# Performance work log

Hardware: AMD Instinct MI355X
Metric: run time of the kernel (lower is better)

Reference implementation:

```python
import jax, jax.numpy as jnp
import numpy as np

N = 100000       # nodes
E = 1600000      # edges (avg degree 16)
D = 128          # features_dim = hidden_dim = out_dim
G = 3            # group_num
NUM = 50000      # nodes present in all time groups
ALPHA = 0.2      # LeakyReLU slope
W_SCALE = 0.05


def setup_inputs() -> dict:
    key = jax.random.key(0)
    ks = jax.random.split(key, 8)
    x = jax.random.normal(ks[0], (N, D), jnp.float32)
    edge_index = jax.random.randint(ks[1], (2, E), 0, N, dtype=jnp.int64)
    past = jax.random.normal(ks[2], (G - 1, NUM, D), jnp.float32)
    W1 = jax.random.normal(ks[3], (2 * D, D), jnp.float32) * W_SCALE
    W2 = jax.random.normal(ks[4], (2 * D, D), jnp.float32) * W_SCALE
    W0 = jax.random.normal(ks[5], (D, D), jnp.float32) * W_SCALE
    Wp = jax.random.normal(ks[6], (G - 1, D, D), jnp.float32) * W_SCALE
    W_T = jax.random.normal(ks[7], (2 * D, D), jnp.float32) * W_SCALE
    return {"x": x, "past": past, "W1": W1, "W2": W2, "W0": W0,
            "Wp": Wp, "W_T": W_T, "edge_index": edge_index, "num": NUM}


def reference(x, past, W1, W2, W0, Wp, W_T, edge_index, num):
    src, dst = edge_index[0], edge_index[1]
    n = x.shape[0]
    deg = jax.ops.segment_sum(jnp.ones(src.shape[0], x.dtype), dst, num_segments=n)
    deg = jnp.maximum(deg, 1.0)[:, None]

    def sage_layer(h, W):
        # mean-aggregate neighbors, concat with self, linear + ReLU
        agg = jax.ops.segment_sum(h[src], dst, num_segments=n) / deg
        return jax.nn.relu(jnp.concatenate([h, agg], axis=1) @ W)

    feat = sage_layer(x, W1)      # [N, D]
    feat = sage_layer(feat, W2)   # [N, D]

    # temporal mean aggregation (dropout is identity in eval mode)
    time_feat = (feat[:num] @ W0 + jnp.einsum('knd,kde->ne', past, Wp)) / G
    fused = jnp.concatenate([feat[:num], time_feat], axis=1) @ W_T  # [num, D]
    f = jax.nn.leaky_relu(fused, ALPHA)
    f = f / jnp.maximum(jnp.linalg.norm(f, axis=1, keepdims=True), 1e-12)
    return jnp.concatenate([f, feat[num:]], axis=0)  # [N, D]
```

## Files before the change

### kernel.cpp

```cpp
#include <hip/hip_runtime.h>

#define FD 128
#define CAP 64
#define BSH 8
#define MAXNB 512

typedef __attribute__((ext_vector_type(8))) short bf16x8;
typedef __attribute__((ext_vector_type(4))) float f32x4;

__device__ __forceinline__ float bflo(unsigned v) { return __uint_as_float(v << 16); }
__device__ __forceinline__ float bfhi(unsigned v) { return __uint_as_float(v & 0xffff0000u); }
__device__ __forceinline__ unsigned short f2b(float f) {
  unsigned u = __float_as_uint(f);
  return (unsigned short)((u + 0x7fffu + ((u >> 16) & 1u)) >> 16);
}
__device__ __forceinline__ unsigned pack2(float x, float y) {
  return (unsigned)f2b(x) | ((unsigned)f2b(y) << 16);
}

#if __has_builtin(__builtin_amdgcn_fdot2_f32_bf16)
#define HAVE_DOT2 1
typedef __attribute__((ext_vector_type(2))) __bf16 bf16x2;
__device__ __forceinline__ float dot2acc(unsigned v, unsigned w, float acc) {
  return __builtin_amdgcn_fdot2_f32_bf16(__builtin_bit_cast(bf16x2, v),
                                         __builtin_bit_cast(bf16x2, w), acc, false);
}
#endif

__global__ __launch_bounds__(256) void k_hist(const int* __restrict__ dst,
                                              int* __restrict__ binCnt, int E, int n, int NB) {
  __shared__ int lh[MAXNB];
  for (int i = threadIdx.x; i < NB; i += 256) lh[i] = 0;
  __syncthreads();
  for (int e = blockIdx.x * 256 + threadIdx.x; e < E; e += gridDim.x * 256) {
    unsigned d = (unsigned)dst[e];
    if (d < (unsigned)n) atomicAdd(&lh[d >> BSH], 1);
  }
  __syncthreads();
  for (int i = threadIdx.x; i < NB; i += 256) {
    int c = lh[i];
    if (c) atomicAdd(&binCnt[i], c);
  }
}

__global__ __launch_bounds__(512) void k_scan(const int* __restrict__ binCnt,
                                              int* __restrict__ binStart,
                                              int* __restrict__ binCur, int NB) {
  __shared__ int buf[512];
  int t = threadIdx.x;
  int v0 = (t < NB) ? binCnt[t] : 0;
  buf[t] = v0;
  __syncthreads();
  for (int off = 1; off < 512; off <<= 1) {
    int v = (t >= off) ? buf[t - off] : 0;
    __syncthreads();
    buf[t] += v;
    __syncthreads();
  }
  if (t < NB) {
    int ex = buf[t] - v0;
    binStart[t] = ex;
    binCur[t] = ex;
  }
}

__global__ __launch_bounds__(256) void k_binscatter(const int* __restrict__ src,
                                                    const int* __restrict__ dst,
                                                    int* __restrict__ binCur,
                                                    unsigned* __restrict__ binned, int E, int n, int NB) {
  __shared__ int lcnt[MAXNB], lbase[MAXNB];
  const int CH = 4096;
  int e0 = blockIdx.x * CH;
  for (int i = threadIdx.x; i < NB; i += 256) lcnt[i] = 0;
  __syncthreads();
  int se[16], de[16];
#pragma unroll
  for (int k = 0; k < 16; ++k) {
    int e = e0 + k * 256 + threadIdx.x;
    int ok = e < E;
    unsigned s = ok ? (unsigned)src[e] : 0u;
    unsigned d = ok ? (unsigned)dst[e] : 0u;
    if (s >= (unsigned)n) s = 0;
    ok = ok && d < (unsigned)n;
    se[k] = (int)s;
    de[k] = ok ? (int)d : -1;
    if (ok) atomicAdd(&lcnt[d >> BSH], 1);
  }
  __syncthreads();
  for (int i = threadIdx.x; i < NB; i += 256) {
    int c = lcnt[i];
    lbase[i] = c ? atomicAdd(&binCur[i], c) : 0;
    lcnt[i] = 0;
  }
  __syncthreads();
#pragma unroll
  for (int k = 0; k < 16; ++k) {
    if (de[k] >= 0) {
      int b = de[k] >> BSH;
      int p = lbase[b] + atomicAdd(&lcnt[b], 1);
      binned[p] = ((unsigned)(de[k] & 255) << 24) | (unsigned)se[k];
    }
  }
}

__global__ __launch_bounds__(256) void k_bucket2(const unsigned* __restrict__ binned,
                                                 const int* __restrict__ binStart,
                                                 const int* __restrict__ binCnt,
                                                 int* __restrict__ cnt,
                                                 int* __restrict__ idx, int n) {
  __shared__ int lcnt[256];
  int bin = blockIdx.x;
  int base = bin << BSH;
  lcnt[threadIdx.x] = 0;
  __syncthreads();
  int s0 = binStart[bin], c0 = binCnt[bin];
  for (int i = threadIdx.x; i < c0; i += 256) {
    unsigned pr = binned[s0 + i];
    int dlow = (int)(pr >> 24);
    int p = atomicAdd(&lcnt[dlow], 1);
    if (p < CAP) idx[(size_t)(base + dlow) * CAP + p] = (int)(pr & 0xFFFFFFu);
  }
  __syncthreads();
  int d = base + threadIdx.x;
  if (d < n) cnt[d] = lcnt[threadIdx.x];
}

__global__ __launch_bounds__(256) void k_xcast(const float4* __restrict__ x,
                                               unsigned short* __restrict__ xb, int total4) {
  int i = blockIdx.x * 256 + threadIdx.x;
  if (i >= total4) return;
  float4 v = x[i];
  *(uint2*)&xb[(size_t)i * 4] = make_uint2(pack2(v.x, v.y), pack2(v.z, v.w));
}

__global__ __launch_bounds__(64) void k_wpack(const float* __restrict__ W,
                                              unsigned short* __restrict__ Wf, int KROWS) {
  int nkt = KROWS >> 5;
  int ct = blockIdx.x % 8, kt = blockIdx.x / 8;
  int lane = threadIdx.x;
  int m = lane & 15, q = lane >> 4;
  int nn = ct * 16 + m;
  int k0 = kt * 32 + q * 8;
  unsigned short tmp[8];
#pragma unroll
  for (int j = 0; j < 8; ++j) tmp[j] = f2b(W[(size_t)(k0 + j) * FD + nn]);
  unsigned short* dst = Wf + ((size_t)(ct * nkt + kt) * 64 + lane) * 8;
  *(uint4*)dst = *(uint4*)tmp;
}

__global__ __launch_bounds__(64) void k_wpack3(const float* __restrict__ W0,
                                               const float* __restrict__ WpA,
                                               const float* __restrict__ WpB,
                                               unsigned short* __restrict__ Wf) {
  int ct = blockIdx.x % 8, kt = blockIdx.x / 8;
  const float* src = kt < 4 ? W0 : (kt < 8 ? WpA : WpB);
  int ktl = kt & 3;
  int lane = threadIdx.x;
  int m = lane & 15, q = lane >> 4;
  int nn = ct * 16 + m;
  int k0 = ktl * 32 + q * 8;
  unsigned short tmp[8];
#pragma unroll
  for (int j = 0; j < 8; ++j) tmp[j] = f2b(src[(size_t)(k0 + j) * FD + nn]);
  unsigned short* dst = Wf + ((size_t)(ct * 12 + kt) * 64 + lane) * 8;
  *(uint4*)dst = *(uint4*)tmp;
}

__global__ __launch_bounds__(256) void k_sage(const unsigned* __restrict__ hb,
                                              const int* __restrict__ cnt,
                                              const int* __restrict__ idx,
                                              const unsigned short* __restrict__ Wf,
                                              float* __restrict__ outf,
                                              unsigned short* __restrict__ outb,
                                              int nbThr, int n) {
  __shared__ unsigned short sa[32][264];
  int tid = threadIdx.x;
  int lane = tid & 63, wv = tid >> 6;
  int rowBase = blockIdx.x * 32;

  for (int i = tid; i < 32 * 32; i += 256) {
    int r = i >> 5, cp = i & 31;
    int gr = rowBase + r;
    uint2 v = (gr < n) ? *(const uint2*)&hb[(size_t)gr * 64 + cp * 2] : make_uint2(0u, 0u);
    *(uint2*)&sa[r][cp * 4] = v;
  }

  int rbase = wv * 8;
  const int* ip = idx + (size_t)(rowBase + rbase) * CAP;
  int vidx[8];
  int c[8];
  int maxc = 0;
#pragma unroll
  for (int j = 0; j < 8; ++j) {
    int gr = rowBase + rbase + j;
    int cj = (gr < n) ? min(cnt[gr], CAP) : 0;
    cj = __builtin_amdgcn_readfirstlane(cj);
    c[j] = cj;
    maxc = max(maxc, cj);
    int v = 0;
    if (lane < cj) v = ip[j * CAP + lane];
    vidx[j] = v;
  }

#ifdef HAVE_DOT2
  float sxa[8], dxa[8];
#pragma unroll
  for (int j = 0; j < 8; ++j) { sxa[j] = 0.f; dxa[j] = 0.f; }
  const unsigned ONES = 0x3F803F80u;
  const unsigned PMON = 0xBF803F80u;

  for (int e = 0; e < maxc; e += 4) {
    int l1 = min(e + 1, CAP - 1), l2 = min(e + 2, CAP - 1), l3 = min(e + 3, CAP - 1);
    unsigned v[8][4];
#pragma unroll
    for (int j = 0; j < 8; ++j) {
      int s0 = __builtin_amdgcn_readlane(vidx[j], e);
      int s1 = __builtin_amdgcn_readlane(vidx[j], l1);
      int s2 = __builtin_amdgcn_readlane(vidx[j], l2);
      int s3 = __builtin_amdgcn_readlane(vidx[j], l3);
      s0 = (e     < c[j]) ? s0 : n;
      s1 = (e + 1 < c[j]) ? s1 : n;
      s2 = (e + 2 < c[j]) ? s2 : n;
      s3 = (e + 3 < c[j]) ? s3 : n;
      v[j][0] = hb[(size_t)s0 * 64 + lane];
      v[j][1] = hb[(size_t)s1 * 64 + lane];
      v[j][2] = hb[(size_t)s2 * 64 + lane];
      v[j][3] = hb[(size_t)s3 * 64 + lane];
    }
#pragma unroll
    for (int j = 0; j < 8; ++j) {
#pragma unroll
      for (int k = 0; k < 4; ++k) {
        sxa[j] = dot2acc(v[j][k], ONES, sxa[j]);
        dxa[j] = dot2acc(v[j][k], PMON, dxa[j]);
      }
    }
  }
#pragma unroll
  for (int j = 0; j < 8; ++j) {
    float inv = 0.5f / fmaxf((float)c[j], 1.0f);
    float ax = (sxa[j] + dxa[j]) * inv;
    float ay = (sxa[j] - dxa[j]) * inv;
    *(unsigned*)&sa[rbase + j][FD + lane * 2] = pack2(ax, ay);
  }
#else
  float ax[8], ay[8];
#pragma unroll
  for (int j = 0; j < 8; ++j) { ax[j] = 0.f; ay[j] = 0.f; }

  for (int e = 0; e < maxc; e += 4) {
    int l1 = min(e + 1, CAP - 1), l2 = min(e + 2, CAP - 1), l3 = min(e + 3, CAP - 1);
    unsigned v[8][4];
#pragma unroll
    for (int j = 0; j < 8; ++j) {
      int s0 = __builtin_amdgcn_readlane(vidx[j], e);
      int s1 = __builtin_amdgcn_readlane(vidx[j], l1);
      int s2 = __builtin_amdgcn_readlane(vidx[j], l2);
      int s3 = __builtin_amdgcn_readlane(vidx[j], l3);
      s0 = (e     < c[j]) ? s0 : n;
      s1 = (e + 1 < c[j]) ? s1 : n;
      s2 = (e + 2 < c[j]) ? s2 : n;
      s3 = (e + 3 < c[j]) ? s3 : n;
      v[j][0] = hb[(size_t)s0 * 64 + lane];
      v[j][1] = hb[(size_t)s1 * 64 + lane];
      v[j][2] = hb[(size_t)s2 * 64 + lane];
      v[j][3] = hb[(size_t)s3 * 64 + lane];
    }
#pragma unroll
    for (int j = 0; j < 8; ++j) {
#pragma unroll
      for (int k = 0; k < 4; ++k) {
        ax[j] += bflo(v[j][k]);
        ay[j] += bfhi(v[j][k]);
      }
    }
  }
#pragma unroll
  for (int j = 0; j < 8; ++j) {
    float inv = 1.0f / fmaxf((float)c[j], 1.0f);
    *(unsigned*)&sa[rbase + j][FD + lane * 2] = pack2(ax[j] * inv, ay[j] * inv);
  }
#endif
  __syncthreads();

  int m = lane & 15, q = lane >> 4;
  f32x4 z = {0.f, 0.f, 0.f, 0.f};
  f32x4 acc[2][2] = {{z, z}, {z, z}};
  int ct0 = wv * 2;
  const bf16x8* WfV = (const bf16x8*)Wf;
#pragma unroll
  for (int kt = 0; kt < 8; ++kt) {
    bf16x8 a0 = *(const bf16x8*)&sa[m][kt * 32 + q * 8];
    bf16x8 a1 = *(const bf16x8*)&sa[16 + m][kt * 32 + q * 8];
    bf16x8 b0 = WfV[(size_t)(ct0 * 8 + kt) * 64 + lane];
    bf16x8 b1 = WfV[(size_t)((ct0 + 1) * 8 + kt) * 64 + lane];
    acc[0][0] = __builtin_amdgcn_mfma_f32_16x16x32_bf16(a0, b0, acc[0][0], 0, 0, 0);
    acc[0][1] = __builtin_amdgcn_mfma_f32_16x16x32_bf16(a0, b1, acc[0][1], 0, 0, 0);
    acc[1][0] = __builtin_amdgcn_mfma_f32_16x16x32_bf16(a1, b0, acc[1][0], 0, 0, 0);
    acc[1][1] = __builtin_amdgcn_mfma_f32_16x16x32_bf16(a1, b1, acc[1][1], 0, 0, 0);
  }

#pragma unroll
  for (int rt = 0; rt < 2; ++rt) {
#pragma unroll
    for (int t = 0; t < 2; ++t) {
      int col = (ct0 + t) * 16 + m;
#pragma unroll
      for (int reg = 0; reg < 4; ++reg) {
        int gr = rowBase + rt * 16 + q * 4 + reg;
        if (gr < n) {
          float v = fmaxf(acc[rt][t][reg], 0.f);
          if (gr < nbThr)
            outb[(size_t)gr * FD + col] = f2b(v);
          else
            outf[(size_t)gr * FD + col] = v;
        }
      }
    }
  }
}

__global__ __launch_bounds__(256) void k_fuse(const unsigned short* __restrict__ feat2b,
                                              const float* __restrict__ past,
                                              const unsigned short* __restrict__ Wcf,
                                              const unsigned short* __restrict__ Wtf,
                                              float* __restrict__ out, int num) {
  __shared__ unsigned short sa[32][392];
  __shared__ float so[32][132];
  int tid = threadIdx.x;
  int lane = tid & 63, wv = tid >> 6;
  int base = blockIdx.x * 32;

  const unsigned* f2u = (const unsigned*)feat2b;
  for (int i = tid; i < 32 * 64; i += 256) {
    int r = i >> 6, cp = i & 63;
    int gr = base + r;
    unsigned uvf = 0u;
    float2 v0 = {0.f, 0.f}, v1 = {0.f, 0.f};
    if (gr < num) {
      uvf = f2u[(size_t)gr * 64 + cp];
      v0 = *(const float2*)&past[(size_t)gr * FD + cp * 2];
      v1 = *(const float2*)&past[(size_t)num * FD + (size_t)gr * FD + cp * 2];
    }
    *(unsigned*)&sa[r][cp * 2]       = uvf;
    *(unsigned*)&sa[r][FD + cp * 2]  = pack2(v0.x, v0.y);
    *(unsigned*)&sa[r][256 + cp * 2] = pack2(v1.x, v1.y);
  }
  __syncthreads();

  int m = lane & 15, q = lane >> 4;
  int ct0 = wv * 2;
  f32x4 z = {0.f, 0.f, 0.f, 0.f};
  const bf16x8* WcV = (const bf16x8*)Wcf;
  const bf16x8* WtV = (const bf16x8*)Wtf;

  f32x4 acc[2][2] = {{z, z}, {z, z}};
#pragma unroll
  for (int kt = 0; kt < 12; ++kt) {
    bf16x8 a0 = *(const bf16x8*)&sa[m][kt * 32 + q * 8];
    bf16x8 a1 = *(const bf16x8*)&sa[16 + m][kt * 32 + q * 8];
    bf16x8 b0 = WcV[(size_t)(ct0 * 12 + kt) * 64 + lane];
    bf16x8 b1 = WcV[(size_t)((ct0 + 1) * 12 + kt) * 64 + lane];
    acc[0][0] = __builtin_amdgcn_mfma_f32_16x16x32_bf16(a0, b0, acc[0][0], 0, 0, 0);
    acc[0][1] = __builtin_amdgcn_mfma_f32_16x16x32_bf16(a0, b1, acc[0][1], 0, 0, 0);
    acc[1][0] = __builtin_amdgcn_mfma_f32_16x16x32_bf16(a1, b0, acc[1][0], 0, 0, 0);
    acc[1][1] = __builtin_amdgcn_mfma_f32_16x16x32_bf16(a1, b1, acc[1][1], 0, 0, 0);
  }
  __syncthreads();

  const float inv3 = 1.0f / 3.0f;
#pragma unroll
  for (int rt = 0; rt < 2; ++rt)
#pragma unroll
    for (int t = 0; t < 2; ++t) {
      int col = (ct0 + t) * 16 + m;
#pragma unroll
      for (int reg = 0; reg < 4; ++reg)
        sa[rt * 16 + q * 4 + reg][FD + col] = f2b(acc[rt][t][reg] * inv3);
    }
  __syncthreads();

  f32x4 acc2[2][2] = {{z, z}, {z, z}};
#pragma unroll
  for (int kt = 0; kt < 8; ++kt) {
    bf16x8 a0 = *(const bf16x8*)&sa[m][kt * 32 + q * 8];
    bf16x8 a1 = *(const bf16x8*)&sa[16 + m][kt * 32 + q * 8];
    bf16x8 b0 = WtV[(size_t)(ct0 * 8 + kt) * 64 + lane];
    bf16x8 b1 = WtV[(size_t)((ct0 + 1) * 8 + kt) * 64 + lane];
    acc2[0][0] = __builtin_amdgcn_mfma_f32_16x16x32_bf16(a0, b0, acc2[0][0], 0, 0, 0);
    acc2[0][1] = __builtin_amdgcn_mfma_f32_16x16x32_bf16(a0, b1, acc2[0][1], 0, 0, 0);
    acc2[1][0] = __builtin_amdgcn_mfma_f32_16x16x32_bf16(a1, b0, acc2[1][0], 0, 0, 0);
    acc2[1][1] = __builtin_amdgcn_mfma_f32_16x16x32_bf16(a1, b1, acc2[1][1], 0, 0, 0);
  }

#pragma unroll
  for (int rt = 0; rt < 2; ++rt)
#pragma unroll
    for (int t = 0; t < 2; ++t) {
      int col = (ct0 + t) * 16 + m;
#pragma unroll
      for (int reg = 0; reg < 4; ++reg) {
        float v = acc2[rt][t][reg];
        so[rt * 16 + q * 4 + reg][col] = v > 0.f ? v : 0.2f * v;
      }
    }
  __syncthreads();

#pragma unroll
  for (int j = 0; j < 8; ++j) {
    int r = wv * 8 + j;
    float v0 = so[r][lane * 2], v1 = so[r][lane * 2 + 1];
    float ss = v0 * v0 + v1 * v1;
#pragma unroll
    for (int mk = 32; mk >= 1; mk >>= 1) ss += __shfl_xor(ss, mk, 64);
    float inv = 1.0f / fmaxf(sqrtf(ss), 1e-12f);
    int gr = base + r;
    if (gr < num) {
      float2 o = {v0 * inv, v1 * inv};
      *(float2*)&out[(size_t)gr * FD + lane * 2] = o;
    }
  }
}

extern "C" void kernel_launch(void* const* d_in, const int* in_sizes, int n_in,
                              void* d_out, int out_size, void* d_ws, size_t ws_size,
                              hipStream_t stream) {
  const float* x    = (const float*)d_in[0];
  const float* past = (const float*)d_in[1];
  const float* W1   = (const float*)d_in[2];
  const float* W2   = (const float*)d_in[3];
  const float* W0   = (const float*)d_in[4];
  const float* Wp   = (const float*)d_in[5];
  const float* WT   = (const float*)d_in[6];
  const int*   ei   = (const int*)d_in[7];

  int N   = in_sizes[0] / FD;
  int NUM = in_sizes[1] / (2 * FD);
  int E   = in_sizes[7] / 2;
  const int* src = ei;
  const int* dst = ei + E;
  float* out = (float*)d_out;

  int NB = (N + 255) >> BSH;

  char* p = (char*)d_ws;
  int* cnt      = (int*)p;  p += (((size_t)N * 4 + 255) & ~(size_t)255);
  int* idx      = (int*)p;  p += (size_t)N * CAP * 4;
  int* binCnt   = (int*)p;  p += MAXNB * 4;
  int* binStart = (int*)p;  p += MAXNB * 4;
  int* binCur   = (int*)p;  p += MAXNB * 4;
  unsigned* binned = (unsigned*)p; p += (size_t)E * 4;
  unsigned short* xb  = (unsigned short*)p; p += (size_t)(N + 1) * FD * 2;
  unsigned short* f1b = (unsigned short*)p; p += (size_t)(N + 1) * FD * 2;
  unsigned short* w1f = (unsigned short*)p; p += (size_t)8 * 8 * 64 * 8 * 2;
  unsigned short* w2f = (unsigned short*)p; p += (size_t)8 * 8 * 64 * 8 * 2;
  unsigned short* wcf = (unsigned short*)p; p += (size_t)8 * 12 * 64 * 8 * 2;
  unsigned short* wtf = (unsigned short*)p;
  unsigned short* f2b = xb;

  hipMemsetAsync(binCnt, 0, MAXNB * sizeof(int), stream);
  hipMemsetAsync(xb + (size_t)N * FD, 0, FD * 2, stream);
  hipMemsetAsync(f1b + (size_t)N * FD, 0, FD * 2, stream);

  k_hist<<<400, 256, 0, stream>>>(dst, binCnt, E, N, NB);
  k_scan<<<1, 512, 0, stream>>>(binCnt, binStart, binCur, NB);
  k_binscatter<<<(E + 4095) / 4096, 256, 0, stream>>>(src, dst, binCur, binned, E, N, NB);
  k_bucket2<<<NB, 256, 0, stream>>>(binned, binStart, binCnt, cnt, idx, N);

  k_xcast<<<(N * 32 + 255) / 256, 256, 0, stream>>>((const float4*)x, xb, N * 32);
  k_wpack<<<64, 64, 0, stream>>>(W1, w1f, 2 * FD);
  k_wpack<<<64, 64, 0, stream>>>(W2, w2f, 2 * FD);
  k_wpack3<<<96, 64, 0, stream>>>(W0, Wp, Wp + FD * FD, wcf);
  k_wpack<<<64, 64, 0, stream>>>(WT, wtf, 2 * FD);

  int sageGrid = (N + 31) / 32;
  k_sage<<<sageGrid, 256, 0, stream>>>((const unsigned*)xb, cnt, idx, w1f, nullptr, f1b, N, N);
  k_sage<<<sageGrid, 256, 0, stream>>>((const unsigned*)f1b, cnt, idx, w2f, out, f2b, NUM, N);
  k_fuse<<<(NUM + 31) / 32, 256, 0, stream>>>(f2b, past, wcf, wtf, out, NUM);
}
```

Before: 400.4 us.

## Merge preprocessing kernels and fold bin scan into scatter and bucket kernels

Merges the x-to-bf16 cast, the destination histogram, all weight packing and the padding-row zeroing into one multi-role prep kernel, replacing several small launches and two memsets. The separate scan kernel is removed: each binscatter and bucket block recomputes the prefix sum of bin counts in shared memory. Bin size grows from 256 to 512 destinations, halving the number of bins and changing the packed edge encoding to a 9-bit local id. This cuts launch count and serialization gaps, at the cost of redundant per-block scans and fewer, larger bucket blocks.

```diff
diff --git a/kernel.cpp b/kernel.cpp
--- a/kernel.cpp
+++ b/kernel.cpp
@@ -2,8 +2,9 @@
 
 #define FD 128
 #define CAP 64
-#define BSH 8
-#define MAXNB 512
+#define BSH 9
+#define BINSZ 512
+#define NBMAX 256
 
 typedef __attribute__((ext_vector_type(8))) short bf16x8;
 typedef __attribute__((ext_vector_type(4))) float f32x4;
@@ -27,56 +28,115 @@
 }
 #endif
 
-__global__ __launch_bounds__(256) void k_hist(const int* __restrict__ dst,
-                                              int* __restrict__ binCnt, int E, int n, int NB) {
-  __shared__ int lh[MAXNB];
-  for (int i = threadIdx.x; i < NB; i += 256) lh[i] = 0;
-  __syncthreads();
-  for (int e = blockIdx.x * 256 + threadIdx.x; e < E; e += gridDim.x * 256) {
-    unsigned d = (unsigned)dst[e];
-    if (d < (unsigned)n) atomicAdd(&lh[d >> BSH], 1);
-  }
-  __syncthreads();
-  for (int i = threadIdx.x; i < NB; i += 256) {
-    int c = lh[i];
-    if (c) atomicAdd(&binCnt[i], c);
-  }
-}
-
-__global__ __launch_bounds__(512) void k_scan(const int* __restrict__ binCnt,
-                                              int* __restrict__ binStart,
-                                              int* __restrict__ binCur, int NB) {
-  __shared__ int buf[512];
+__device__ __forceinline__ void wpack_tile(const float* __restrict__ W,
+                                           unsigned short* __restrict__ Wf,
+                                           int nkt, int tt, int lane) {
+  int ct = tt & 7, kt = tt >> 3;
+  int m = lane & 15, q = lane >> 4;
+  int nn = ct * 16 + m;
+  int k0 = kt * 32 + q * 8;
+  unsigned short tmp[8];
+#pragma unroll
+  for (int j = 0; j < 8; ++j) tmp[j] = f2b(W[(size_t)(k0 + j) * FD + nn]);
+  unsigned short* dst = Wf + ((size_t)(ct * nkt + kt) * 64 + lane) * 8;
+  *(uint4*)dst = *(uint4*)tmp;
+}
+
+__global__ __launch_bounds__(256) void k_prep(const float4* __restrict__ x4,
+                                              unsigned short* __restrict__ xb, int total4,
+                                              const int* __restrict__ dst,
+                                              int* __restrict__ binCnt, int E, int n, int NB,
+                                              const float* __restrict__ W1,
+                                              const float* __restrict__ W2,
+                                              const float* __restrict__ W0,
+                                              const float* __restrict__ Wp,
+                                              const float* __restrict__ WT,
+                                              unsigned short* __restrict__ w1f,
+                                              unsigned short* __restrict__ w2f,
+                                              unsigned short* __restrict__ wcf,
+                                              unsigned short* __restrict__ wtf,
+                                              unsigned short* __restrict__ f1b,
+                                              int XCB, int HB) {
+  __shared__ int lh[NBMAX];
+  int b = blockIdx.x, tid = threadIdx.x;
+
+  if (b < XCB) {
+    int i = b * 256 + tid;
+    if (i < total4) {
+      float4 v = x4[i];
+      *(uint2*)&xb[(size_t)i * 4] = make_uint2(pack2(v.x, v.y), pack2(v.z, v.w));
+    }
+    return;
+  }
+  b -= XCB;
+  if (b < HB) {
+    for (int i = tid; i < NB; i += 256) lh[i] = 0;
+    __syncthreads();
+    for (int e = b * 256 + tid; e < E; e += HB * 256) {
+      unsigned d = (unsigned)dst[e];
+      if (d < (unsigned)n) atomicAdd(&lh[d >> BSH], 1);
+    }
+    __syncthreads();
+    for (int i = tid; i < NB; i += 256) {
+      int c = lh[i];
+      if (c) atomicAdd(&binCnt[i], c);
+    }
+    return;
+  }
+  b -= HB;
+  if (b < 72) {
+    int t4 = b * 4 + (tid >> 6);
+    int lane = tid & 63;
+    if (t4 < 64) wpack_tile(W1, w1f, 8, t4, lane);
+    else if (t4 < 128) wpack_tile(W2, w2f, 8, t4 - 64, lane);
+    else if (t4 < 192) wpack_tile(WT, wtf, 8, t4 - 128, lane);
+    else {
+      int tt = t4 - 192;
+      int ct = tt & 7, kt = tt >> 3;
+      const float* src = kt < 4 ? W0 : (kt < 8 ? Wp : (Wp + FD * FD));
+      int ktl = kt & 3;
+      int m = lane & 15, q = lane >> 4;
+      int nn = ct * 16 + m;
+      int k0 = ktl * 32 + q * 8;
+      unsigned short tmp[8];
+#pragma unroll
+      for (int j = 0; j < 8; ++j) tmp[j] = f2b(src[(size_t)(k0 + j) * FD + nn]);
+      unsigned short* dstp = wcf + ((size_t)(ct * 12 + kt) * 64 + lane) * 8;
+      *(uint4*)dstp = *(uint4*)tmp;
+    }
+    return;
+  }
+  if (tid < 64) ((unsigned*)&xb[(size_t)n * FD])[tid] = 0u;
+  else if (tid < 128) ((unsigned*)&f1b[(size_t)n * FD])[tid - 64] = 0u;
+}
+
+__global__ __launch_bounds__(256) void k_binscatter(const int* __restrict__ src,
+                                                    const int* __restrict__ dst,
+                                                    const int* __restrict__ binCnt,
+                                                    int* __restrict__ binCur,
+                                                    unsigned* __restrict__ binned,
+                                                    int E, int n, int NB) {
+  __shared__ int sbuf[NBMAX], sstart[NBMAX], lcnt[NBMAX], lbase[NBMAX];
   int t = threadIdx.x;
   int v0 = (t < NB) ? binCnt[t] : 0;
-  buf[t] = v0;
-  __syncthreads();
-  for (int off = 1; off < 512; off <<= 1) {
-    int v = (t >= off) ? buf[t - off] : 0;
+  sbuf[t] = v0;
+  __syncthreads();
+  for (int off = 1; off < 256; off <<= 1) {
+    int v = (t >= off) ? sbuf[t - off] : 0;
     __syncthreads();
-    buf[t] += v;
+    sbuf[t] += v;
     __syncthreads();
   }
-  if (t < NB) {
-    int ex = buf[t] - v0;
-    binStart[t] = ex;
-    binCur[t] = ex;
-  }
-}
-
-__global__ __launch_bounds__(256) void k_binscatter(const int* __restrict__ src,
-                                                    const int* __restrict__ dst,
-                                                    int* __restrict__ binCur,
-                                                    unsigned* __restrict__ binned, int E, int n, int NB) {
-  __shared__ int lcnt[MAXNB], lbase[MAXNB];
+  sstart[t] = sbuf[t] - v0;
+  lcnt[t] = 0;
+  __syncthreads();
+
   const int CH = 4096;
   int e0 = blockIdx.x * CH;
-  for (int i = threadIdx.x; i < NB; i += 256) lcnt[i] = 0;
-  __syncthreads();
   int se[16], de[16];
 #pragma unroll
   for (int k = 0; k < 16; ++k) {
-    int e = e0 + k * 256 + threadIdx.x;
+    int e = e0 + k * 256 + t;
     int ok = e < E;
     unsigned s = ok ? (unsigned)src[e] : 0u;
     unsigned d = ok ? (unsigned)dst[e] : 0u;
@@ -87,83 +147,56 @@
     if (ok) atomicAdd(&lcnt[d >> BSH], 1);
   }
   __syncthreads();
-  for (int i = threadIdx.x; i < NB; i += 256) {
+  for (int i = t; i < NB; i += 256) {
     int c = lcnt[i];
-    lbase[i] = c ? atomicAdd(&binCur[i], c) : 0;
+    lbase[i] = c ? (sstart[i] + atomicAdd(&binCur[i], c)) : 0;
     lcnt[i] = 0;
   }
   __syncthreads();
 #pragma unroll
   for (int k = 0; k < 16; ++k) {
     if (de[k] >= 0) {
-      int b = de[k] >> BSH;
-      int p = lbase[b] + atomicAdd(&lcnt[b], 1);
-      binned[p] = ((unsigned)(de[k] & 255) << 24) | (unsigned)se[k];
+      int bb = de[k] >> BSH;
+      int p = lbase[bb] + atomicAdd(&lcnt[bb], 1);
+      binned[p] = ((unsigned)(de[k] & (BINSZ - 1)) << 23) | (unsigned)se[k];
     }
   }
 }
 
 __global__ __launch_bounds__(256) void k_bucket2(const unsigned* __restrict__ binned,
-                                                 const int* __restrict__ binStart,
                                                  const int* __restrict__ binCnt,
                                                  int* __restrict__ cnt,
-                                                 int* __restrict__ idx, int n) {
-  __shared__ int lcnt[256];
-  int bin = blockIdx.x;
+                                                 int* __restrict__ idx, int n, int NB) {
+  __shared__ int sbuf[NBMAX];
+  __shared__ int lcnt[BINSZ];
+  int bin = blockIdx.x, t = threadIdx.x;
+  int v0 = (t < NB) ? binCnt[t] : 0;
+  sbuf[t] = v0;
+  __syncthreads();
+  for (int off = 1; off < 256; off <<= 1) {
+    int v = (t >= off) ? sbuf[t - off] : 0;
+    __syncthreads();
+    sbuf[t] += v;
+    __syncthreads();
+  }
+  int c0 = binCnt[bin];
+  int s0 = sbuf[bin] - c0;
+  lcnt[t] = 0;
+  lcnt[t + 256] = 0;
+  __syncthreads();
+
   int base = bin << BSH;
-  lcnt[threadIdx.x] = 0;
-  __syncthreads();
-  int s0 = binStart[bin], c0 = binCnt[bin];
-  for (int i = threadIdx.x; i < c0; i += 256) {
+  for (int i = t; i < c0; i += 256) {
     unsigned pr = binned[s0 + i];
-    int dlow = (int)(pr >> 24);
+    int dlow = (int)(pr >> 23);
     int p = atomicAdd(&lcnt[dlow], 1);
-    if (p < CAP) idx[(size_t)(base + dlow) * CAP + p] = (int)(pr & 0xFFFFFFu);
-  }
-  __syncthreads();
-  int d = base + threadIdx.x;
-  if (d < n) cnt[d] = lcnt[threadIdx.x];
-}
-
-__global__ __launch_bounds__(256) void k_xcast(const float4* __restrict__ x,
-                                               unsigned short* __restrict__ xb, int total4) {
-  int i = blockIdx.x * 256 + threadIdx.x;
-  if (i >= total4) return;
-  float4 v = x[i];
-  *(uint2*)&xb[(size_t)i * 4] = make_uint2(pack2(v.x, v.y), pack2(v.z, v.w));
-}
-
-__global__ __launch_bounds__(64) void k_wpack(const float* __restrict__ W,
-                                              unsigned short* __restrict__ Wf, int KROWS) {
-  int nkt = KROWS >> 5;
-  int ct = blockIdx.x % 8, kt = blockIdx.x / 8;
-  int lane = threadIdx.x;
-  int m = lane & 15, q = lane >> 4;
-  int nn = ct * 16 + m;
-  int k0 = kt * 32 + q * 8;
-  unsigned short tmp[8];
-#pragma unroll
-  for (int j = 0; j < 8; ++j) tmp[j] = f2b(W[(size_t)(k0 + j) * FD + nn]);
-  unsigned short* dst = Wf + ((size_t)(ct * nkt + kt) * 64 + lane) * 8;
-  *(uint4*)dst = *(uint4*)tmp;
-}
-
-__global__ __launch_bounds__(64) void k_wpack3(const float* __restrict__ W0,
-                                               const float* __restrict__ WpA,
-                                               const float* __restrict__ WpB,
-                                               unsigned short* __restrict__ Wf) {
-  int ct = blockIdx.x % 8, kt = blockIdx.x / 8;
-  const float* src = kt < 4 ? W0 : (kt < 8 ? WpA : WpB);
-  int ktl = kt & 3;
-  int lane = threadIdx.x;
-  int m = lane & 15, q = lane >> 4;
-  int nn = ct * 16 + m;
-  int k0 = ktl * 32 + q * 8;
-  unsigned short tmp[8];
-#pragma unroll
-  for (int j = 0; j < 8; ++j) tmp[j] = f2b(src[(size_t)(k0 + j) * FD + nn]);
-  unsigned short* dst = Wf + ((size_t)(ct * 12 + kt) * 64 + lane) * 8;
-  *(uint4*)dst = *(uint4*)tmp;
+    if (p < CAP) idx[(size_t)(base + dlow) * CAP + p] = (int)(pr & 0x7FFFFFu);
+  }
+  __syncthreads();
+  for (int d0 = t; d0 < BINSZ; d0 += 256) {
+    int d = base + d0;
+    if (d < n) cnt[d] = lcnt[d0];
+  }
 }
 
 __global__ __launch_bounds__(256) void k_sage(const unsigned* __restrict__ hb,
@@ -201,6 +234,7 @@
     if (lane < cj) v = ip[j * CAP + lane];
     vidx[j] = v;
   }
+  maxc = min(maxc, CAP);
 
 #ifdef HAVE_DOT2
   float sxa[8], dxa[8];
@@ -441,14 +475,13 @@
   const int* dst = ei + E;
   float* out = (float*)d_out;
 
-  int NB = (N + 255) >> BSH;
+  int NB = (N + BINSZ - 1) >> BSH;
 
   char* p = (char*)d_ws;
   int* cnt      = (int*)p;  p += (((size_t)N * 4 + 255) & ~(size_t)255);
   int* idx      = (int*)p;  p += (size_t)N * CAP * 4;
-  int* binCnt   = (int*)p;  p += MAXNB * 4;
-  int* binStart = (int*)p;  p += MAXNB * 4;
-  int* binCur   = (int*)p;  p += MAXNB * 4;
+  int* binCnt   = (int*)p;  p += NBMAX * 4;
+  int* binCur   = (int*)p;  p += NBMAX * 4;
   unsigned* binned = (unsigned*)p; p += (size_t)E * 4;
   unsigned short* xb  = (unsigned short*)p; p += (size_t)(N + 1) * FD * 2;
   unsigned short* f1b = (unsigned short*)p; p += (size_t)(N + 1) * FD * 2;
@@ -456,25 +489,23 @@
   unsigned short* w2f = (unsigned short*)p; p += (size_t)8 * 8 * 64 * 8 * 2;
   unsigned short* wcf = (unsigned short*)p; p += (size_t)8 * 12 * 64 * 8 * 2;
   unsigned short* wtf = (unsigned short*)p;
-  unsigned short* f2b = xb;
-
-  hipMemsetAsync(binCnt, 0, MAXNB * sizeof(int), stream);
-  hipMemsetAsync(xb + (size_t)N * FD, 0, FD * 2, stream);
-  hipMemsetAsync(f1b + (size_t)N * FD, 0, FD * 2, stream);
-
-  k_hist<<<400, 256, 0, stream>>>(dst, binCnt, E, N, NB);
-  k_scan<<<1, 512, 0, stream>>>(binCnt, binStart, binCur, NB);
-  k_binscatter<<<(E + 4095) / 4096, 256, 0, stream>>>(src, dst, binCur, binned, E, N, NB);
-  k_bucket2<<<NB, 256, 0, stream>>>(binned, binStart, binCnt, cnt, idx, N);
-
-  k_xcast<<<(N * 32 + 255) / 256, 256, 0, stream>>>((const float4*)x, xb, N * 32);
-  k_wpack<<<64, 64, 0, stream>>>(W1, w1f, 2 * FD);
-  k_wpack<<<64, 64, 0, stream>>>(W2, w2f, 2 * FD);
-  k_wpack3<<<96, 64, 0, stream>>>(W0, Wp, Wp + FD * FD, wcf);
-  k_wpack<<<64, 64, 0, stream>>>(WT, wtf, 2 * FD);
+  unsigned short* f2b_buf = xb;
+
+  hipMemsetAsync(binCnt, 0, 2 * NBMAX * sizeof(int), stream);
+
+  int total4 = N * 32;
+  int XCB = (total4 + 255) / 256;
+  int HB  = 400;
+  k_prep<<<XCB + HB + 72 + 1, 256, 0, stream>>>((const float4*)x, xb, total4,
+                                                dst, binCnt, E, N, NB,
+                                                W1, W2, W0, Wp, WT,
+                                                w1f, w2f, wcf, wtf, f1b, XCB, HB);
+
+  k_binscatter<<<(E + 4095) / 4096, 256, 0, stream>>>(src, dst, binCnt, binCur, binned, E, N, NB);
+  k_bucket2<<<NB, 256, 0, stream>>>(binned, binCnt, cnt, idx, N, NB);
 
   int sageGrid = (N + 31) / 32;
   k_sage<<<sageGrid, 256, 0, stream>>>((const unsigned*)xb, cnt, idx, w1f, nullptr, f1b, N, N);
-  k_sage<<<sageGrid, 256, 0, stream>>>((const unsigned*)f1b, cnt, idx, w2f, out, f2b, NUM, N);
-  k_fuse<<<(NUM + 31) / 32, 256, 0, stream>>>(f2b, past, wcf, wtf, out, NUM);
-}
+  k_sage<<<sageGrid, 256, 0, stream>>>((const unsigned*)f1b, cnt, idx, w2f, out, f2b_buf, NUM, N);
+  k_fuse<<<(NUM + 31) / 32, 256, 0, stream>>>(f2b_buf, past, wcf, wtf, out, NUM);
+}
```

New measurement: 388.2 us. 3.1% less time.
